# Kernel tuning notes

Hardware: AMD Instinct MI355X
Metric: run time of the kernel (lower is better)

Reference implementation:

```python
import jax, jax.numpy as jnp
import numpy as np

B, R, H, Q, D = 16, 400, 8, 64, 1200  # BatchSize, ROIs, heads, q, BOLDs
THRESH_INIT = 0.01

def setup_inputs() -> dict:
    key = jax.random.key(0)
    k1, k2, k3, k4, k5 = jax.random.split(key, 5)
    s = 1.0 / np.sqrt(D)
    return {
        "x": jax.random.normal(k1, (B, R, D), dtype=jnp.float32),
        "Wq": jax.random.normal(k2, (D, H * Q), dtype=jnp.float32) * s,
        "bq": jax.random.normal(k3, (H * Q,), dtype=jnp.float32) * 0.01,
        "Wk": jax.random.normal(k4, (D, H * Q), dtype=jnp.float32) * s,
        "bk": jax.random.normal(k5, (H * Q,), dtype=jnp.float32) * 0.01,
        "threshold": jnp.ones((), dtype=jnp.float32),
    }

def reference(x, Wq, bq, Wk, bk, threshold):
    # Q,K projections: [B,R,H*Q] -> [B,R,H,Q]
    q = (x @ Wq + bq).reshape(B, R, H, Q)
    k = (x @ Wk + bk).reshape(B, R, H, Q)
    # QK^T per head: [B,H,R,R]
    rel = jnp.einsum("bihq,bjhq->bhij", q, k) / jnp.float32(Q)
    rel = jax.nn.softmax(rel, axis=-1)
    # threshold-subtract + relu sparsification (learned scalar, init 0.01)
    rel = jax.nn.relu(rel - threshold * THRESH_INIT)
    return rel
```

## Files before the change

### kernel.cpp

```cpp
#include <hip/hip_runtime.h>
#include <stdint.h>

#define DPAD 1216
#define MROWS 6400

typedef float f32x4 __attribute__((ext_vector_type(4)));
typedef __bf16 bf16x8 __attribute__((ext_vector_type(8)));
typedef __attribute__((address_space(3))) uint8_t as3_u8;
typedef __attribute__((address_space(1))) uint8_t as1_u8;

__device__ __forceinline__ void gload_lds16(const void* g, void* l) {
  __builtin_amdgcn_global_load_lds((as1_u8*)g, (as3_u8*)l, 16, 0, 0);
}

__global__ void cvt_fused(const float* __restrict__ x,
                          const float* __restrict__ wq, const float* __restrict__ wk,
                          __bf16* __restrict__ xb, __bf16* __restrict__ wt) {
  if (blockIdx.x < 3800) {
    const int id = blockIdx.x * 256 + threadIdx.x;
    const int row = id / 152;
    const int c = id - row * 152;
    const int col = c * 8;
    bf16x8 v;
    if (col < 1200) {
      const float4* p = (const float4*)(x + row * 1200 + col);
      const float4 f0 = p[0], f1 = p[1];
      v[0] = (__bf16)f0.x; v[1] = (__bf16)f0.y; v[2] = (__bf16)f0.z; v[3] = (__bf16)f0.w;
      v[4] = (__bf16)f1.x; v[5] = (__bf16)f1.y; v[6] = (__bf16)f1.z; v[7] = (__bf16)f1.w;
    } else {
#pragma unroll
      for (int i = 0; i < 8; ++i) v[i] = (__bf16)0.0f;
    }
    *(bf16x8*)(xb + (size_t)row * DPAD + col) = v;
  } else {
    const int id = (blockIdx.x - 3800) * 256 + threadIdx.x;
    const int n = id / 152;
    const int c = id - n * 152;
    const int k0 = c * 8;
    const float* src = (n < 512) ? (wq + n) : (wk + (n - 512));
    bf16x8 v;
#pragma unroll
    for (int i = 0; i < 8; ++i) {
      const int k = k0 + i;
      v[i] = (k < 1200) ? (__bf16)src[(size_t)k * 512] : (__bf16)0.0f;
    }
    *(bf16x8*)(wt + (size_t)n * DPAD + k0) = v;
  }
}

__global__ __launch_bounds__(256, 3) void gemm_qk(const __bf16* __restrict__ xb,
                                                  const __bf16* __restrict__ wt,
                                                  const float* __restrict__ bq,
                                                  const float* __restrict__ bk,
                                                  __bf16* __restrict__ qk) {
  __shared__ __bf16 As[128 * 64];
  __shared__ __bf16 Bs[128 * 64];
  const int bid = blockIdx.x;
  const int wg = (bid & 7) * 50 + (bid >> 3);
  const int n0 = (wg / 50) * 128;
  const int m0 = (wg % 50) * 128;
  const int t = threadIdx.x;
  const int lane = t & 63;
  const int wid = t >> 6;
  const int wr = wid >> 1, wc = wid & 1;
  const int lrow = lane & 15, lk = lane >> 4;

  f32x4 acc[4][4];
#pragma unroll
  for (int i = 0; i < 4; ++i)
#pragma unroll
    for (int j = 0; j < 4; ++j) acc[i][j] = (f32x4){0.f, 0.f, 0.f, 0.f};

  for (int k0 = 0; k0 < DPAD; k0 += 64) {
#pragma unroll
    for (int it = 0; it < 4; ++it) {
      const int id = it * 256 + t;
      const int row = id >> 3, cc = id & 7;
      gload_lds16(xb + (size_t)(m0 + row) * DPAD + k0 + cc * 8, (char*)As + id * 16);
      gload_lds16(wt + (size_t)(n0 + row) * DPAD + k0 + cc * 8, (char*)Bs + id * 16);
    }
    __syncthreads();
#pragma unroll
    for (int kk = 0; kk < 2; ++kk) {
      bf16x8 a[4], bfr[4];
#pragma unroll
      for (int i = 0; i < 4; ++i)
        a[i] = *(const bf16x8*)(As + (wr * 64 + i * 16 + lrow) * 64 + kk * 32 + lk * 8);
#pragma unroll
      for (int i = 0; i < 4; ++i)
        bfr[i] = *(const bf16x8*)(Bs + (wc * 64 + i * 16 + lrow) * 64 + kk * 32 + lk * 8);
#pragma unroll
      for (int mi = 0; mi < 4; ++mi)
#pragma unroll
        for (int ni = 0; ni < 4; ++ni)
          acc[mi][ni] = __builtin_amdgcn_mfma_f32_16x16x32_bf16(a[mi], bfr[ni], acc[mi][ni], 0, 0, 0);
    }
    __syncthreads();
  }
#pragma unroll
  for (int mi = 0; mi < 4; ++mi) {
#pragma unroll
    for (int ni = 0; ni < 4; ++ni) {
      const int gr0 = m0 + wr * 64 + mi * 16 + lk * 4;
      const int gc = n0 + wc * 64 + ni * 16 + lrow;
      const float bias = (gc < 512) ? bq[gc] : bk[gc - 512];
#pragma unroll
      for (int r = 0; r < 4; ++r)
        qk[(size_t)(gr0 + r) * 1024 + gc] = (__bf16)(acc[mi][ni][r] + bias);
    }
  }
}

__global__ __launch_bounds__(256) void attn(const __bf16* __restrict__ qk,
                                            const float* __restrict__ thr_p,
                                            float* __restrict__ out) {
  __shared__ float slds[16 * 400];
  const int bh = blockIdx.y;
  const int b = bh >> 3;
  const int h = bh & 7;
  const int r0 = blockIdx.x * 16;
  const int t = threadIdx.x;
  const int lane = t & 63;
  const int wid = t >> 6;
  const int lrow = lane & 15, lk = lane >> 4;
  const __bf16* kbase = qk + (size_t)(b * 400) * 1024 + 512 + h * 64;
  const __bf16* qbase = qk + (size_t)(b * 400 + r0) * 1024 + h * 64;

  bf16x8 aq[2];
#pragma unroll
  for (int kk = 0; kk < 2; ++kk)
    aq[kk] = *(const bf16x8*)(qbase + (size_t)lrow * 1024 + kk * 32 + lk * 8);

  for (int jt = wid; jt < 25; jt += 4) {
    f32x4 acc = (f32x4){0.f, 0.f, 0.f, 0.f};
#pragma unroll
    for (int kk = 0; kk < 2; ++kk) {
      const bf16x8 bkf = *(const bf16x8*)(kbase + (size_t)(jt * 16 + lrow) * 1024 + kk * 32 + lk * 8);
      acc = __builtin_amdgcn_mfma_f32_16x16x32_bf16(aq[kk], bkf, acc, 0, 0, 0);
    }
    const int scol = jt * 16 + lrow;
#pragma unroll
    for (int r = 0; r < 4; ++r)
      slds[(lk * 4 + r) * 400 + scol] = acc[r] * 0.015625f;
  }
  __syncthreads();

  const int row = t >> 4, c = t & 15;
  const float thr = thr_p[0] * 0.01f;
  float vals[25];
  float m = -1e30f;
#pragma unroll
  for (int j = 0; j < 25; ++j) {
    vals[j] = slds[row * 400 + j * 16 + c];
    m = fmaxf(m, vals[j]);
  }
#pragma unroll
  for (int off = 8; off >= 1; off >>= 1) m = fmaxf(m, __shfl_xor(m, off, 16));
  float sum = 0.f;
#pragma unroll
  for (int j = 0; j < 25; ++j) {
    vals[j] = __expf(vals[j] - m);
    sum += vals[j];
  }
#pragma unroll
  for (int off = 8; off >= 1; off >>= 1) sum += __shfl_xor(sum, off, 16);
  const float inv = 1.0f / sum;
  float* orow = out + ((size_t)bh * 400 + r0 + row) * 400;
#pragma unroll
  for (int j = 0; j < 25; ++j) {
    const float p = vals[j] * inv - thr;
    orow[j * 16 + c] = p > 0.f ? p : 0.f;
  }
}

extern "C" void kernel_launch(void* const* d_in, const int* in_sizes, int n_in,
                              void* d_out, int out_size, void* d_ws, size_t ws_size,
                              hipStream_t stream) {
  const float* x   = (const float*)d_in[0];
  const float* Wq  = (const float*)d_in[1];
  const float* bq  = (const float*)d_in[2];
  const float* Wk  = (const float*)d_in[3];
  const float* bk  = (const float*)d_in[4];
  const float* thr = (const float*)d_in[5];
  char* ws = (char*)d_ws;
  __bf16* xb = (__bf16*)ws;
  __bf16* wt = (__bf16*)(ws + 15564800);
  __bf16* qk = (__bf16*)(ws + 18055168);
  float* out = (float*)d_out;

  cvt_fused<<<dim3(4408), dim3(256), 0, stream>>>(x, Wq, Wk, xb, wt);
  gemm_qk<<<dim3(400), dim3(256), 0, stream>>>(xb, wt, bq, bk, qk);
  attn<<<dim3(25, 128), dim3(256), 0, stream>>>(qk, thr, out);
}
```

Measured before the change: 84.43 us.

## Switch projection and attention GEMMs to FP8 inputs and stage output through LDS

Converts x, the weights and the intermediate Q/K buffer from bf16 to FP8 (e4m3) and uses the fp8 MFMA instructions in both the projection GEMM and the QK^T step. This halves workspace traffic and doubles the math rate per instruction, with the K-step tile cut to 32. The attention epilogue also writes the thresholded softmax back to LDS and stores it with coalesced float4 writes. The cost is a large loss of precision in Q/K and in the logits, which could break the accuracy tolerance.

```diff
diff --git a/kernel.cpp b/kernel.cpp
--- a/kernel.cpp
+++ b/kernel.cpp
@@ -2,10 +2,8 @@
 #include <stdint.h>
 
 #define DPAD 1216
-#define MROWS 6400
 
 typedef float f32x4 __attribute__((ext_vector_type(4)));
-typedef __bf16 bf16x8 __attribute__((ext_vector_type(8)));
 typedef __attribute__((address_space(3))) uint8_t as3_u8;
 typedef __attribute__((address_space(1))) uint8_t as1_u8;
 
@@ -13,48 +11,54 @@
   __builtin_amdgcn_global_load_lds((as1_u8*)g, (as3_u8*)l, 16, 0, 0);
 }
 
+__device__ __forceinline__ long pack_fp8x8(const float* f) {
+  int w0 = __builtin_amdgcn_cvt_pk_fp8_f32(f[0], f[1], 0, false);
+  w0 = __builtin_amdgcn_cvt_pk_fp8_f32(f[2], f[3], w0, true);
+  int w1 = __builtin_amdgcn_cvt_pk_fp8_f32(f[4], f[5], 0, false);
+  w1 = __builtin_amdgcn_cvt_pk_fp8_f32(f[6], f[7], w1, true);
+  return (long)(((unsigned long)(unsigned)w1 << 32) | (unsigned)w0);
+}
+
 __global__ void cvt_fused(const float* __restrict__ x,
                           const float* __restrict__ wq, const float* __restrict__ wk,
-                          __bf16* __restrict__ xb, __bf16* __restrict__ wt) {
+                          uint8_t* __restrict__ x8, uint8_t* __restrict__ w8) {
   if (blockIdx.x < 3800) {
     const int id = blockIdx.x * 256 + threadIdx.x;
     const int row = id / 152;
     const int c = id - row * 152;
     const int col = c * 8;
-    bf16x8 v;
+    float f[8];
     if (col < 1200) {
       const float4* p = (const float4*)(x + row * 1200 + col);
-      const float4 f0 = p[0], f1 = p[1];
-      v[0] = (__bf16)f0.x; v[1] = (__bf16)f0.y; v[2] = (__bf16)f0.z; v[3] = (__bf16)f0.w;
-      v[4] = (__bf16)f1.x; v[5] = (__bf16)f1.y; v[6] = (__bf16)f1.z; v[7] = (__bf16)f1.w;
+      const float4 a = p[0], b = p[1];
+      f[0] = a.x; f[1] = a.y; f[2] = a.z; f[3] = a.w;
+      f[4] = b.x; f[5] = b.y; f[6] = b.z; f[7] = b.w;
     } else {
 #pragma unroll
-      for (int i = 0; i < 8; ++i) v[i] = (__bf16)0.0f;
+      for (int i = 0; i < 8; ++i) f[i] = 0.f;
     }
-    *(bf16x8*)(xb + (size_t)row * DPAD + col) = v;
+    *(long*)(x8 + (size_t)row * DPAD + col) = pack_fp8x8(f);
   } else {
     const int id = (blockIdx.x - 3800) * 256 + threadIdx.x;
     const int n = id / 152;
     const int c = id - n * 152;
     const int k0 = c * 8;
     const float* src = (n < 512) ? (wq + n) : (wk + (n - 512));
-    bf16x8 v;
+    float f[8];
 #pragma unroll
-    for (int i = 0; i < 8; ++i) {
-      const int k = k0 + i;
-      v[i] = (k < 1200) ? (__bf16)src[(size_t)k * 512] : (__bf16)0.0f;
-    }
-    *(bf16x8*)(wt + (size_t)n * DPAD + k0) = v;
+    for (int i = 0; i < 8; ++i)
+      f[i] = (k0 + i < 1200) ? src[(size_t)(k0 + i) * 512] : 0.f;
+    *(long*)(w8 + (size_t)n * DPAD + k0) = pack_fp8x8(f);
   }
 }
 
-__global__ __launch_bounds__(256, 3) void gemm_qk(const __bf16* __restrict__ xb,
-                                                  const __bf16* __restrict__ wt,
-                                                  const float* __restrict__ bq,
-                                                  const float* __restrict__ bk,
-                                                  __bf16* __restrict__ qk) {
-  __shared__ __bf16 As[128 * 64];
-  __shared__ __bf16 Bs[128 * 64];
+__global__ __launch_bounds__(256) void gemm_qk(const uint8_t* __restrict__ x8,
+                                               const uint8_t* __restrict__ w8,
+                                               const float* __restrict__ bq,
+                                               const float* __restrict__ bk,
+                                               uint8_t* __restrict__ qk8) {
+  __shared__ uint8_t As[128 * 32];
+  __shared__ uint8_t Bs[128 * 32];
   const int bid = blockIdx.x;
   const int wg = (bid & 7) * 50 + (bid >> 3);
   const int n0 = (wg / 50) * 128;
@@ -71,30 +75,23 @@
 #pragma unroll
     for (int j = 0; j < 4; ++j) acc[i][j] = (f32x4){0.f, 0.f, 0.f, 0.f};
 
-  for (int k0 = 0; k0 < DPAD; k0 += 64) {
+  const int srow = t >> 1, scc = t & 1;
+  for (int k0 = 0; k0 < DPAD; k0 += 32) {
+    gload_lds16(x8 + (size_t)(m0 + srow) * DPAD + k0 + scc * 16, (char*)As + t * 16);
+    gload_lds16(w8 + (size_t)(n0 + srow) * DPAD + k0 + scc * 16, (char*)Bs + t * 16);
+    __syncthreads();
+    long a[4], bfr[4];
 #pragma unroll
-    for (int it = 0; it < 4; ++it) {
-      const int id = it * 256 + t;
-      const int row = id >> 3, cc = id & 7;
-      gload_lds16(xb + (size_t)(m0 + row) * DPAD + k0 + cc * 8, (char*)As + id * 16);
-      gload_lds16(wt + (size_t)(n0 + row) * DPAD + k0 + cc * 8, (char*)Bs + id * 16);
-    }
-    __syncthreads();
+    for (int i = 0; i < 4; ++i)
+      a[i] = *(const long*)(As + (wr * 64 + i * 16 + lrow) * 32 + lk * 8);
 #pragma unroll
-    for (int kk = 0; kk < 2; ++kk) {
-      bf16x8 a[4], bfr[4];
+    for (int i = 0; i < 4; ++i)
+      bfr[i] = *(const long*)(Bs + (wc * 64 + i * 16 + lrow) * 32 + lk * 8);
 #pragma unroll
-      for (int i = 0; i < 4; ++i)
-        a[i] = *(const bf16x8*)(As + (wr * 64 + i * 16 + lrow) * 64 + kk * 32 + lk * 8);
+    for (int mi = 0; mi < 4; ++mi)
 #pragma unroll
-      for (int i = 0; i < 4; ++i)
-        bfr[i] = *(const bf16x8*)(Bs + (wc * 64 + i * 16 + lrow) * 64 + kk * 32 + lk * 8);
-#pragma unroll
-      for (int mi = 0; mi < 4; ++mi)
-#pragma unroll
-        for (int ni = 0; ni < 4; ++ni)
-          acc[mi][ni] = __builtin_amdgcn_mfma_f32_16x16x32_bf16(a[mi], bfr[ni], acc[mi][ni], 0, 0, 0);
-    }
+      for (int ni = 0; ni < 4; ++ni)
+        acc[mi][ni] = __builtin_amdgcn_mfma_f32_16x16x32_fp8_fp8(a[mi], bfr[ni], acc[mi][ni], 0, 0, 0);
     __syncthreads();
   }
 #pragma unroll
@@ -105,13 +102,16 @@
       const int gc = n0 + wc * 64 + ni * 16 + lrow;
       const float bias = (gc < 512) ? bq[gc] : bk[gc - 512];
 #pragma unroll
-      for (int r = 0; r < 4; ++r)
-        qk[(size_t)(gr0 + r) * 1024 + gc] = (__bf16)(acc[mi][ni][r] + bias);
+      for (int r = 0; r < 4; ++r) {
+        const float v = acc[mi][ni][r] + bias;
+        const int pk = __builtin_amdgcn_cvt_pk_fp8_f32(v, v, 0, false);
+        qk8[(size_t)(gr0 + r) * 1024 + gc] = (uint8_t)(pk & 0xff);
+      }
     }
   }
 }
 
-__global__ __launch_bounds__(256) void attn(const __bf16* __restrict__ qk,
+__global__ __launch_bounds__(256) void attn(const uint8_t* __restrict__ qk8,
                                             const float* __restrict__ thr_p,
                                             float* __restrict__ out) {
   __shared__ float slds[16 * 400];
@@ -123,20 +123,20 @@
   const int lane = t & 63;
   const int wid = t >> 6;
   const int lrow = lane & 15, lk = lane >> 4;
-  const __bf16* kbase = qk + (size_t)(b * 400) * 1024 + 512 + h * 64;
-  const __bf16* qbase = qk + (size_t)(b * 400 + r0) * 1024 + h * 64;
+  const uint8_t* kbase = qk8 + (size_t)(b * 400) * 1024 + 512 + h * 64;
+  const uint8_t* qbase = qk8 + (size_t)(b * 400 + r0) * 1024 + h * 64;
 
-  bf16x8 aq[2];
+  long aq[2];
 #pragma unroll
   for (int kk = 0; kk < 2; ++kk)
-    aq[kk] = *(const bf16x8*)(qbase + (size_t)lrow * 1024 + kk * 32 + lk * 8);
+    aq[kk] = *(const long*)(qbase + (size_t)lrow * 1024 + kk * 32 + lk * 8);
 
   for (int jt = wid; jt < 25; jt += 4) {
     f32x4 acc = (f32x4){0.f, 0.f, 0.f, 0.f};
 #pragma unroll
     for (int kk = 0; kk < 2; ++kk) {
-      const bf16x8 bkf = *(const bf16x8*)(kbase + (size_t)(jt * 16 + lrow) * 1024 + kk * 32 + lk * 8);
-      acc = __builtin_amdgcn_mfma_f32_16x16x32_bf16(aq[kk], bkf, acc, 0, 0, 0);
+      const long bkf = *(const long*)(kbase + (size_t)(jt * 16 + lrow) * 1024 + kk * 32 + lk * 8);
+      acc = __builtin_amdgcn_mfma_f32_16x16x32_fp8_fp8(aq[kk], bkf, acc, 0, 0, 0);
     }
     const int scol = jt * 16 + lrow;
 #pragma unroll
@@ -165,12 +165,14 @@
 #pragma unroll
   for (int off = 8; off >= 1; off >>= 1) sum += __shfl_xor(sum, off, 16);
   const float inv = 1.0f / sum;
-  float* orow = out + ((size_t)bh * 400 + r0 + row) * 400;
 #pragma unroll
-  for (int j = 0; j < 25; ++j) {
-    const float p = vals[j] * inv - thr;
-    orow[j * 16 + c] = p > 0.f ? p : 0.f;
-  }
+  for (int j = 0; j < 25; ++j)
+    slds[row * 400 + j * 16 + c] = fmaxf(vals[j] * inv - thr, 0.f);
+  __syncthreads();
+
+  float* obase = out + ((size_t)bh * 400 + r0) * 400;
+  for (int i = t; i < 1600; i += 256)
+    *(float4*)(obase + 4 * i) = *(const float4*)(slds + 4 * i);
 }
 
 extern "C" void kernel_launch(void* const* d_in, const int* in_sizes, int n_in,
@@ -183,12 +185,12 @@
   const float* bk  = (const float*)d_in[4];
   const float* thr = (const float*)d_in[5];
   char* ws = (char*)d_ws;
-  __bf16* xb = (__bf16*)ws;
-  __bf16* wt = (__bf16*)(ws + 15564800);
-  __bf16* qk = (__bf16*)(ws + 18055168);
+  uint8_t* x8  = (uint8_t*)ws;
+  uint8_t* w8  = (uint8_t*)(ws + 7782400);
+  uint8_t* qk8 = (uint8_t*)(ws + 9027584);
   float* out = (float*)d_out;
 
-  cvt_fused<<<dim3(4408), dim3(256), 0, stream>>>(x, Wq, Wk, xb, wt);
-  gemm_qk<<<dim3(400), dim3(256), 0, stream>>>(xb, wt, bq, bk, qk);
-  attn<<<dim3(25, 128), dim3(256), 0, stream>>>(qk, thr, out);
+  cvt_fused<<<dim3(4408), dim3(256), 0, stream>>>(x, Wq, Wk, x8, w8);
+  gemm_qk<<<dim3(400), dim3(256), 0, stream>>>(x8, w8, bq, bk, qk8);
+  attn<<<dim3(25, 128), dim3(256), 0, stream>>>(qk8, thr, out);
 }
```

New measurement: 85.97 us. Within noise of the previous version (+1.8%).
